# Optimization experiments

Hardware: AMD Instinct MI355X
Metric: run time of the kernel (lower is better)

The kernel has to match this reference:

```python
import jax, jax.numpy as jnp
import numpy as np

BN_EPS = 1e-5

def conv1x1(x, w, b):
    # x: [B,C,H,W], w: [O,C], b: [O] -> [B,O,H,W]
    return jnp.einsum('bchw,oc->bohw', x, w) + b[None, :, None, None]

def maxpool2x2(x):
    B, C, H, W = x.shape
    return x.reshape(B, C, H // 2, 2, W // 2, 2).max(axis=(3, 5))

def setup_inputs() -> dict:
    key = jax.random.key(0)
    ks = jax.random.split(key, 8)
    B, C, Ci, H, W = 16, 256, 128, 64, 64
    s_in = np.sqrt(2.0 / C).astype(np.float32)   # kaiming fan_out-ish scale
    s_out = np.sqrt(2.0 / Ci).astype(np.float32)
    return {
        'inp0': jax.random.normal(ks[0], (1,), jnp.float32),
        'x': jax.random.normal(ks[1], (B, C, H, W), jnp.float32),
        'g_w': jax.random.normal(ks[2], (Ci, C), jnp.float32) * s_in,
        'g_b': jnp.zeros((Ci,), jnp.float32),
        'theta_w': jax.random.normal(ks[3], (Ci, C), jnp.float32) * s_in,
        'theta_b': jnp.zeros((Ci,), jnp.float32),
        'phi_w': jax.random.normal(ks[4], (Ci, C), jnp.float32) * s_in,
        'phi_b': jnp.zeros((Ci,), jnp.float32),
        'W_w': jax.random.normal(ks[5], (C, Ci), jnp.float32) * s_out,
        'W_b': jnp.zeros((C,), jnp.float32),
        'bn_gamma': jnp.ones((C,), jnp.float32),
        'bn_beta': jnp.zeros((C,), jnp.float32),
    }

def reference(inp0, x, g_w, g_b, theta_w, theta_b, phi_w, phi_b, W_w, W_b, bn_gamma, bn_beta):
    B, C, H, W = x.shape
    Ci = g_w.shape[0]
    # g and phi are conv1x1 followed by 2x2 maxpool (sub_sample=True)
    g_x = maxpool2x2(conv1x1(x, g_w, g_b)).reshape(B, Ci, -1)        # [B,Ci,N']
    g_x = g_x.transpose(0, 2, 1)                                      # [B,N',Ci]
    theta_x = conv1x1(x, theta_w, theta_b).reshape(B, Ci, -1)         # [B,Ci,N]
    theta_x = theta_x.transpose(0, 2, 1)                              # [B,N,Ci]
    phi_x = maxpool2x2(conv1x1(x, phi_w, phi_b)).reshape(B, Ci, -1)   # [B,Ci,N']
    f = jnp.einsum('bnc,bcm->bnm', theta_x, phi_x)                    # [B,N,N'] (no scaling)
    f_div_C = jax.nn.softmax(f, axis=-1)
    y = jnp.einsum('bnm,bmc->bnc', f_div_C, g_x)                      # [B,N,Ci]
    y = y.transpose(0, 2, 1).reshape(B, Ci, H, W)
    W_y = conv1x1(y, W_w, W_b)                                        # [B,C,H,W]
    # BatchNorm2d in training mode: batch statistics (biased var), eps=1e-5
    mean = W_y.mean(axis=(0, 2, 3))
    var = W_y.var(axis=(0, 2, 3))
    W_y = (W_y - mean[None, :, None, None]) * jax.lax.rsqrt(var + BN_EPS)[None, :, None, None]
    W_y = W_y * bn_gamma[None, :, None, None] + bn_beta[None, :, None, None]
    z = W_y + x
    # original returns list(inputs[:index]) + [z] + list(inputs[index+1:])
    return (inp0, z)
```

## Files before the change

### kernel.cpp

```cpp
#include <hip/hip_runtime.h>
#include <stdint.h>

typedef __attribute__((ext_vector_type(4))) float f32x4;
typedef __attribute__((ext_vector_type(8))) short s16x8;

__device__ __forceinline__ unsigned short bf16_rne(float f) {
    union { float f; unsigned u; } v; v.f = f;
    return (unsigned short)((v.u + 0x7fffu + ((v.u >> 16) & 1u)) >> 16);
}
__device__ __forceinline__ float bf16_to_f32(unsigned short h) {
    union { unsigned u; float f; } v; v.u = ((unsigned)h) << 16;
    return v.f;
}

__device__ __forceinline__ void async_copy16(unsigned short* lds, const unsigned short* glb) {
    __builtin_amdgcn_global_load_lds(
        (const __attribute__((address_space(1))) unsigned int*)(glb),
        (__attribute__((address_space(3))) unsigned int*)(lds),
        16, 0, 0);
}


template<int MODE>
__global__ __launch_bounds__(256) void conv_kernel(
    const float* __restrict__ x,
    const float* __restrict__ w,
    const float* __restrict__ bias,
    unsigned short* __restrict__ outH,
    unsigned short* __restrict__ outL)
{
    const int b   = blockIdx.y;
    const int n0  = blockIdx.x * 128;
    const int tid = threadIdx.x;
    const int wv  = tid >> 6;
    const int l   = tid & 63;
    const int lg  = l >> 4;
    const int lc  = l & 15;

    __shared__ __align__(16) unsigned short Ah[128][40];
    __shared__ __align__(16) unsigned short Al[128][40];

    f32x4 acc[8][2];
#pragma unroll
    for (int i = 0; i < 8; i++)
#pragma unroll
        for (int j = 0; j < 2; j++) acc[i][j] = (f32x4){0.f, 0.f, 0.f, 0.f};

    for (int kc = 0; kc < 256; kc += 32) {
        __syncthreads();
#pragma unroll
        for (int i = 0; i < 16; i++) {
            int lin = i * 256 + tid;
            int cc  = lin >> 7;
            int nn  = lin & 127;
            float v = x[((size_t)b * 256 + (kc + cc)) * 4096 + n0 + nn];
            unsigned short h = bf16_rne(v);
            Ah[nn][cc] = h;
            if (MODE != 2) Al[nn][cc] = bf16_rne(v - bf16_to_f32(h));
        }
        __syncthreads();

        s16x8 wh[2], wl[2];
#pragma unroll
        for (int ot = 0; ot < 2; ot++) {
            int orow = wv * 32 + ot * 16 + lc;
            const float* wp = w + (size_t)orow * 256 + kc + lg * 8;
#pragma unroll
            for (int j = 0; j < 8; j++) {
                float wvv = wp[j];
                unsigned short h = bf16_rne(wvv);
                wh[ot][j] = (short)h;
                if (MODE != 2) wl[ot][j] = (short)bf16_rne(wvv - bf16_to_f32(h));
            }
        }

#pragma unroll
        for (int mt = 0; mt < 8; mt++) {
            s16x8 ah = *(const s16x8*)&Ah[mt * 16 + lc][lg * 8];
            s16x8 al;
            if (MODE != 2) al = *(const s16x8*)&Al[mt * 16 + lc][lg * 8];
#pragma unroll
            for (int ot = 0; ot < 2; ot++) {
                acc[mt][ot] = __builtin_amdgcn_mfma_f32_16x16x32_bf16(ah, wh[ot], acc[mt][ot], 0, 0, 0);
                if (MODE != 2) {
                    acc[mt][ot] = __builtin_amdgcn_mfma_f32_16x16x32_bf16(ah, wl[ot], acc[mt][ot], 0, 0, 0);
                    acc[mt][ot] = __builtin_amdgcn_mfma_f32_16x16x32_bf16(al, wh[ot], acc[mt][ot], 0, 0, 0);
                }
            }
        }
    }

    if (MODE == 0) {
#pragma unroll
        for (int mt = 0; mt < 8; mt++)
#pragma unroll
            for (int ot = 0; ot < 2; ot++) {
                int o = wv * 32 + ot * 16 + lc;
                float bs = bias[o];
#pragma unroll
                for (int r = 0; r < 4; r++) {
                    int n = n0 + mt * 16 + lg * 4 + r;
                    float v = acc[mt][ot][r] + bs;
                    unsigned short h = bf16_rne(v);
                    size_t idx = ((size_t)b * 4096 + n) * 128 + o;
                    outH[idx] = h;
                    outL[idx] = bf16_rne(v - bf16_to_f32(h));
                }
            }
    } else {
        const int mbase = blockIdx.x * 32;
#pragma unroll
        for (int mt = 0; mt < 4; mt++)
#pragma unroll
            for (int ot = 0; ot < 2; ot++) {
                int o = wv * 32 + ot * 16 + lc;
                float bs = bias[o];
#pragma unroll
                for (int pair = 0; pair < 2; pair++) {
                    float v = fmaxf(fmaxf(acc[mt][ot][2 * pair], acc[mt][ot][2 * pair + 1]),
                                    fmaxf(acc[mt + 4][ot][2 * pair], acc[mt + 4][ot][2 * pair + 1])) + bs;
                    int pw = mt * 8 + lg * 2 + pair;
                    int m  = mbase + pw;
                    if (MODE == 1) {
                        unsigned short h = bf16_rne(v);
                        size_t idx = ((size_t)b * 1024 + m) * 128 + o;
                        outH[idx] = h;
                        outL[idx] = bf16_rne(v - bf16_to_f32(h));
                    } else {
                        outH[((size_t)b * 128 + o) * 1024 + m] = bf16_rne(v);
                    }
                }
            }
    }
}

__global__ __launch_bounds__(256, 4) void attn_kernel(
    const unsigned short* __restrict__ thH,
    const unsigned short* __restrict__ thL,
    const unsigned short* __restrict__ phH,
    const unsigned short* __restrict__ phL,
    const unsigned short* __restrict__ gp,
    unsigned short* __restrict__ y)
{
    const int fid  = blockIdx.x + (blockIdx.y << 6);
    const int xcd  = fid & 7;
    const int slot = fid >> 3;
    const int b    = 2 * xcd + (slot >> 6);
    const int n0   = (slot & 63) * 64;

    const int tid = threadIdx.x;
    const int wv  = tid >> 6;
    const int l   = tid & 63;
    const int lg  = l >> 4;
    const int lc  = l & 15;

    __shared__ __align__(16) unsigned short Kh[2][32 * 128];
    __shared__ __align__(16) unsigned short Kl[2][32 * 128];
    __shared__ __align__(16) unsigned short Pb[4][16 * 40];

    const unsigned short* phHb = phH + (size_t)b * 1024 * 128;
    const unsigned short* phLb = phL + (size_t)b * 1024 * 128;
    const unsigned short* gpb  = gp  + (size_t)b * 128 * 1024;
    unsigned short* Pw = Pb[wv];

    s16x8 qh[4], ql[4];
    {
        const size_t qrow = ((size_t)b * 4096 + n0 + wv * 16 + lc) * 128;
#pragma unroll
        for (int ks = 0; ks < 4; ks++) {
            qh[ks] = *(const s16x8*)(thH + qrow + ks * 32 + lg * 8);
            ql[ks] = *(const s16x8*)(thL + qrow + ks * 32 + lg * 8);
        }
    }

    f32x4 O[8];
#pragma unroll
    for (int t = 0; t < 8; t++) O[t] = (f32x4){0.f, 0.f, 0.f, 0.f};
    float mrun[4] = {-1e30f, -1e30f, -1e30f, -1e30f};
    float lrun[4] = {0.f, 0.f, 0.f, 0.f};

    const int lr  = l >> 4;
    const int sc_ = l & 15;

#define STAGE(buf, kt_)                                                              \
    {                                                                                \
        _Pragma("unroll")                                                            \
        for (int t = 0; t < 2; t++) {                                                \
            int Rt = wv * 8 + t * 4;                                                 \
            int R  = Rt + lr;                                                        \
            int ck = sc_ ^ (R & 15);                                                 \
            size_t src = ((size_t)((kt_) * 32 + R)) * 128 + ck * 8;                  \
            async_copy16(&Kh[buf][Rt * 128], phHb + src);                            \
            async_copy16(&Kl[buf][Rt * 128], phLb + src);                            \
        }                                                                            \
    }

    STAGE(0, 0);

    for (int kt = 0; kt < 32; kt++) {
        const int cur = kt & 1;
        __syncthreads();
        if (kt < 31) STAGE(cur ^ 1, kt + 1);

        const unsigned short* KhT = Kh[cur];
        const unsigned short* KlT = Kl[cur];

        f32x4 s[2];
#pragma unroll
        for (int ct = 0; ct < 2; ct++) s[ct] = (f32x4){0.f, 0.f, 0.f, 0.f};
#pragma unroll
        for (int ct = 0; ct < 2; ct++) {
            const int row = ct * 16 + lc;
#pragma unroll
            for (int ks = 0; ks < 4; ks++) {
                const int slt = (ks * 4 + lg) ^ lc;
                s16x8 kh = *(const s16x8*)(KhT + row * 128 + slt * 8);
                s16x8 kl = *(const s16x8*)(KlT + row * 128 + slt * 8);
                s[ct] = __builtin_amdgcn_mfma_f32_16x16x32_bf16(qh[ks], kh, s[ct], 0, 0, 0);
                s[ct] = __builtin_amdgcn_mfma_f32_16x16x32_bf16(qh[ks], kl, s[ct], 0, 0, 0);
                s[ct] = __builtin_amdgcn_mfma_f32_16x16x32_bf16(ql[ks], kh, s[ct], 0, 0, 0);
            }
        }

        float tm[4];
#pragma unroll
        for (int r = 0; r < 4; r++) tm[r] = fmaxf(s[0][r], s[1][r]);
#pragma unroll
        for (int d = 1; d < 16; d <<= 1)
#pragma unroll
            for (int r = 0; r < 4; r++) tm[r] = fmaxf(tm[r], __shfl_xor(tm[r], d, 64));

        bool grow = (tm[0] > mrun[0]) || (tm[1] > mrun[1]) ||
                    (tm[2] > mrun[2]) || (tm[3] > mrun[3]);
        if (__any(grow)) {
            float scv[4];
#pragma unroll
            for (int r = 0; r < 4; r++) {
                float mn = fmaxf(mrun[r], tm[r]);
                scv[r] = __expf(mrun[r] - mn);
                mrun[r] = mn;
                lrun[r] *= scv[r];
            }
#pragma unroll
            for (int t = 0; t < 8; t++)
#pragma unroll
                for (int r = 0; r < 4; r++) O[t][r] *= scv[r];
        }

        float ts[4] = {0.f, 0.f, 0.f, 0.f};
#pragma unroll
        for (int ct = 0; ct < 2; ct++)
#pragma unroll
            for (int r = 0; r < 4; r++) {
                float e = __expf(s[ct][r] - mrun[r]);
                s[ct][r] = e;
                ts[r] += e;
            }
#pragma unroll
        for (int d = 1; d < 16; d <<= 1)
#pragma unroll
            for (int r = 0; r < 4; r++) ts[r] += __shfl_xor(ts[r], d, 64);
#pragma unroll
        for (int r = 0; r < 4; r++) lrun[r] += ts[r];

#pragma unroll
        for (int ct = 0; ct < 2; ct++)
#pragma unroll
            for (int r = 0; r < 4; r++)
                Pw[(lg * 4 + r) * 40 + ct * 16 + lc] = bf16_rne(s[ct][r]);

        const int mt = kt * 32;
        s16x8 pa = *(const s16x8*)(Pw + lc * 40 + lg * 8);
#pragma unroll
        for (int ci_t = 0; ci_t < 8; ci_t++) {
            s16x8 vb = *(const s16x8*)(gpb + (size_t)(ci_t * 16 + lc) * 1024 + mt + lg * 8);
            O[ci_t] = __builtin_amdgcn_mfma_f32_16x16x32_bf16(pa, vb, O[ci_t], 0, 0, 0);
        }
    }

#pragma unroll
    for (int r = 0; r < 4; r++) {
        float inv = 1.0f / lrun[r];
        int n = n0 + wv * 16 + lg * 4 + r;
        size_t base = ((size_t)b * 4096 + n) * 128;
#pragma unroll
        for (int ci_t = 0; ci_t < 8; ci_t++)
            y[base + ci_t * 16 + lc] = bf16_rne(O[ci_t][r] * inv);
    }
#undef STAGE
}

__global__ __launch_bounds__(256) void wconv_kernel(
    const unsigned short* __restrict__ y,
    const float* __restrict__ Ww,
    const float* __restrict__ Wb,
    unsigned short* __restrict__ wy)
{
    const int b   = blockIdx.z;
    const int o0  = blockIdx.x * 64;
    const int nb  = blockIdx.y * 256;
    const int tid = threadIdx.x;
    const int wv  = tid >> 6;
    const int l   = tid & 63;
    const int lg  = l >> 4;
    const int lc  = l & 15;
    const int n0  = nb + wv * 64;

    f32x4 acc[4][4];
#pragma unroll
    for (int i = 0; i < 4; i++)
#pragma unroll
        for (int j = 0; j < 4; j++) acc[i][j] = (f32x4){0.f, 0.f, 0.f, 0.f};

#pragma unroll
    for (int ks = 0; ks < 4; ks++) {
        s16x8 a[4];
#pragma unroll
        for (int ot = 0; ot < 4; ot++) {
            const float* wp = Ww + (size_t)(o0 + ot * 16 + lc) * 128 + ks * 32 + lg * 8;
#pragma unroll
            for (int j = 0; j < 8; j++) a[ot][j] = (short)bf16_rne(wp[j]);
        }
#pragma unroll
        for (int nt = 0; nt < 4; nt++) {
            s16x8 bf = *(const s16x8*)(y + ((size_t)b * 4096 + n0 + nt * 16 + lc) * 128 + ks * 32 + lg * 8);
#pragma unroll
            for (int ot = 0; ot < 4; ot++)
                acc[ot][nt] = __builtin_amdgcn_mfma_f32_16x16x32_bf16(a[ot], bf, acc[ot][nt], 0, 0, 0);
        }
    }
#pragma unroll
    for (int ot = 0; ot < 4; ot++) {
#pragma unroll
        for (int r = 0; r < 4; r++) {
            int o = o0 + ot * 16 + lg * 4 + r;
            float bsv = Wb[o];
#pragma unroll
            for (int nt = 0; nt < 4; nt++) {
                float v = acc[ot][nt][r] + bsv;
                wy[((size_t)b * 256 + o) * 4096 + n0 + nt * 16 + lc] = bf16_rne(v);
            }
        }
    }
}

__global__ __launch_bounds__(256) void stats_kernel(
    const unsigned short* __restrict__ wy,
    const float* __restrict__ gamma, const float* __restrict__ beta,
    float* __restrict__ scale, float* __restrict__ shift)
{
    const int o = blockIdx.x;
    const int t = threadIdx.x;
    float s1 = 0.f, s2 = 0.f;
    for (int b = 0; b < 16; b++) {
        const unsigned short* p = wy + ((size_t)b * 256 + o) * 4096;
#pragma unroll
        for (int i = 0; i < 4; i++) {
            uint2 u = *(const uint2*)(p + i * 1024 + t * 4);
            float v0 = bf16_to_f32((unsigned short)(u.x & 0xffff));
            float v1 = bf16_to_f32((unsigned short)(u.x >> 16));
            float v2 = bf16_to_f32((unsigned short)(u.y & 0xffff));
            float v3 = bf16_to_f32((unsigned short)(u.y >> 16));
            s1 += v0 + v1 + v2 + v3;
            s2 += v0 * v0 + v1 * v1 + v2 * v2 + v3 * v3;
        }
    }
#pragma unroll
    for (int d = 1; d < 64; d <<= 1) { s1 += __shfl_xor(s1, d, 64); s2 += __shfl_xor(s2, d, 64); }
    __shared__ float rs1[4], rs2[4];
    if ((t & 63) == 0) { rs1[t >> 6] = s1; rs2[t >> 6] = s2; }
    __syncthreads();
    if (t == 0) {
        float S1 = rs1[0] + rs1[1] + rs1[2] + rs1[3];
        float S2 = rs2[0] + rs2[1] + rs2[2] + rs2[3];
        const float cnt = 16.0f * 4096.0f;
        float mean = S1 / cnt;
        float var  = S2 / cnt - mean * mean;
        float sc = gamma[o] * rsqrtf(var + 1e-5f);
        scale[o] = sc;
        shift[o] = beta[o] - mean * sc;
    }
}

__global__ __launch_bounds__(256) void final_kernel(
    const unsigned short* __restrict__ wy,
    const float* __restrict__ x,
    const float* __restrict__ scale, const float* __restrict__ shift,
    const float* __restrict__ inp0,
    float* __restrict__ out)
{
    if (blockIdx.x == 0 && threadIdx.x == 0) out[0] = inp0[0];
    float* z = out + 1;
    const size_t total4 = (size_t)16 * 256 * 4096 / 4;
    for (size_t v = (size_t)blockIdx.x * 256 + threadIdx.x; v < total4; v += (size_t)gridDim.x * 256) {
        size_t e = v * 4;
        int c = (int)((e >> 12) & 255);
        uint2 u = *(const uint2*)(wy + e);
        float4 xv = *(const float4*)(x + e);
        float sc = scale[c], sh = shift[c];
        float z0 = sc * bf16_to_f32((unsigned short)(u.x & 0xffff)) + sh + xv.x;
        float z1 = sc * bf16_to_f32((unsigned short)(u.x >> 16))    + sh + xv.y;
        float z2 = sc * bf16_to_f32((unsigned short)(u.y & 0xffff)) + sh + xv.z;
        float z3 = sc * bf16_to_f32((unsigned short)(u.y >> 16))    + sh + xv.w;
        z[e + 0] = z0; z[e + 1] = z1; z[e + 2] = z2; z[e + 3] = z3;
    }
}

extern "C" void kernel_launch(void* const* d_in, const int* in_sizes, int n_in,
                              void* d_out, int out_size, void* d_ws, size_t ws_size,
                              hipStream_t stream) {
    const float* inp0  = (const float*)d_in[0];
    const float* x     = (const float*)d_in[1];
    const float* g_w   = (const float*)d_in[2];
    const float* g_b   = (const float*)d_in[3];
    const float* th_w  = (const float*)d_in[4];
    const float* th_b  = (const float*)d_in[5];
    const float* ph_w  = (const float*)d_in[6];
    const float* ph_b  = (const float*)d_in[7];
    const float* W_w   = (const float*)d_in[8];
    const float* W_b   = (const float*)d_in[9];
    const float* gamma = (const float*)d_in[10];
    const float* beta  = (const float*)d_in[11];

    char* ws = (char*)d_ws;
    const size_t MB = 1048576;
    unsigned short* thH = (unsigned short*)(ws);
    unsigned short* thL = (unsigned short*)(ws + 16 * MB);
    unsigned short* phH = (unsigned short*)(ws + 32 * MB);
    unsigned short* phL = (unsigned short*)(ws + 36 * MB);
    unsigned short* gpv = (unsigned short*)(ws + 40 * MB);
    unsigned short* yv  = (unsigned short*)(ws + 44 * MB);
    unsigned short* wy  = (unsigned short*)(ws + 60 * MB);
    float* scaleb       = (float*)(ws + 92 * MB);
    float* shiftb       = (float*)(ws + 92 * MB + 1024);

    conv_kernel<0><<<dim3(32, 16), 256, 0, stream>>>(x, th_w, th_b, thH, thL);
    conv_kernel<1><<<dim3(32, 16), 256, 0, stream>>>(x, ph_w, ph_b, phH, phL);
    conv_kernel<2><<<dim3(32, 16), 256, 0, stream>>>(x, g_w, g_b, gpv, gpv);
    attn_kernel<<<dim3(64, 16), 256, 0, stream>>>(thH, thL, phH, phL, gpv, yv);
    wconv_kernel<<<dim3(4, 16, 16), 256, 0, stream>>>(yv, W_w, W_b, wy);
    stats_kernel<<<dim3(256), 256, 0, stream>>>(wy, gamma, beta, scaleb, shiftb);
    final_kernel<<<dim3(2048), 256, 0, stream>>>(wy, x, scaleb, shiftb, inp0, (float*)d_out);
}
```

Measured before the change: 418.8 us.

## Transpose score MFMA operands so softmax row reductions need fewer shuffles

New measurement: 402.0 us. 1.04x faster.

```diff
diff --git a/kernel.cpp b/kernel.cpp
--- a/kernel.cpp
+++ b/kernel.cpp
@@ -49,14 +49,20 @@
     for (int kc = 0; kc < 256; kc += 32) {
         __syncthreads();
 #pragma unroll
-        for (int i = 0; i < 16; i++) {
+        for (int i = 0; i < 8; i++) {
             int lin = i * 256 + tid;
-            int cc  = lin >> 7;
+            int cp  = lin >> 7;
             int nn  = lin & 127;
-            float v = x[((size_t)b * 256 + (kc + cc)) * 4096 + n0 + nn];
-            unsigned short h = bf16_rne(v);
-            Ah[nn][cc] = h;
-            if (MODE != 2) Al[nn][cc] = bf16_rne(v - bf16_to_f32(h));
+            const float* xp = x + ((size_t)b * 256 + (kc + 2 * cp)) * 4096 + n0 + nn;
+            float v0 = xp[0];
+            float v1 = xp[4096];
+            unsigned short h0 = bf16_rne(v0), h1 = bf16_rne(v1);
+            *(unsigned*)&Ah[nn][2 * cp] = (unsigned)h0 | ((unsigned)h1 << 16);
+            if (MODE != 2) {
+                unsigned short l0 = bf16_rne(v0 - bf16_to_f32(h0));
+                unsigned short l1 = bf16_rne(v1 - bf16_to_f32(h1));
+                *(unsigned*)&Al[nn][2 * cp] = (unsigned)l0 | ((unsigned)l1 << 16);
+            }
         }
         __syncthreads();
 
@@ -176,8 +182,8 @@
     f32x4 O[8];
 #pragma unroll
     for (int t = 0; t < 8; t++) O[t] = (f32x4){0.f, 0.f, 0.f, 0.f};
-    float mrun[4] = {-1e30f, -1e30f, -1e30f, -1e30f};
-    float lrun[4] = {0.f, 0.f, 0.f, 0.f};
+    float mrun = -1e30f;
+    float lrun = 0.f;
 
     const int lr  = l >> 4;
     const int sc_ = l & 15;
@@ -216,58 +222,52 @@
                 const int slt = (ks * 4 + lg) ^ lc;
                 s16x8 kh = *(const s16x8*)(KhT + row * 128 + slt * 8);
                 s16x8 kl = *(const s16x8*)(KlT + row * 128 + slt * 8);
-                s[ct] = __builtin_amdgcn_mfma_f32_16x16x32_bf16(qh[ks], kh, s[ct], 0, 0, 0);
-                s[ct] = __builtin_amdgcn_mfma_f32_16x16x32_bf16(qh[ks], kl, s[ct], 0, 0, 0);
-                s[ct] = __builtin_amdgcn_mfma_f32_16x16x32_bf16(ql[ks], kh, s[ct], 0, 0, 0);
-            }
-        }
-
-        float tm[4];
-#pragma unroll
-        for (int r = 0; r < 4; r++) tm[r] = fmaxf(s[0][r], s[1][r]);
-#pragma unroll
-        for (int d = 1; d < 16; d <<= 1)
-#pragma unroll
-            for (int r = 0; r < 4; r++) tm[r] = fmaxf(tm[r], __shfl_xor(tm[r], d, 64));
-
-        bool grow = (tm[0] > mrun[0]) || (tm[1] > mrun[1]) ||
-                    (tm[2] > mrun[2]) || (tm[3] > mrun[3]);
-        if (__any(grow)) {
-            float scv[4];
+                s[ct] = __builtin_amdgcn_mfma_f32_16x16x32_bf16(kh, qh[ks], s[ct], 0, 0, 0);
+                s[ct] = __builtin_amdgcn_mfma_f32_16x16x32_bf16(kl, qh[ks], s[ct], 0, 0, 0);
+                s[ct] = __builtin_amdgcn_mfma_f32_16x16x32_bf16(kh, ql[ks], s[ct], 0, 0, 0);
+            }
+        }
+
+        float tm = fmaxf(fmaxf(fmaxf(s[0][0], s[0][1]), fmaxf(s[0][2], s[0][3])),
+                         fmaxf(fmaxf(s[1][0], s[1][1]), fmaxf(s[1][2], s[1][3])));
+        tm = fmaxf(tm, __shfl_xor(tm, 16, 64));
+        tm = fmaxf(tm, __shfl_xor(tm, 32, 64));
+
+        if (__any(tm > mrun)) {
+            float mn  = fmaxf(mrun, tm);
+            float scr = __expf(mrun - mn);
+            mrun = mn;
+            lrun *= scr;
+            float scO[4];
+#pragma unroll
+            for (int r = 0; r < 4; r++) scO[r] = __shfl(scr, lg * 4 + r, 64);
+#pragma unroll
+            for (int t = 0; t < 8; t++)
+#pragma unroll
+                for (int r = 0; r < 4; r++) O[t][r] *= scO[r];
+        }
+
+        float ts = 0.f;
+        float p[8];
+#pragma unroll
+        for (int ct = 0; ct < 2; ct++)
 #pragma unroll
             for (int r = 0; r < 4; r++) {
-                float mn = fmaxf(mrun[r], tm[r]);
-                scv[r] = __expf(mrun[r] - mn);
-                mrun[r] = mn;
-                lrun[r] *= scv[r];
-            }
-#pragma unroll
-            for (int t = 0; t < 8; t++)
-#pragma unroll
-                for (int r = 0; r < 4; r++) O[t][r] *= scv[r];
-        }
-
-        float ts[4] = {0.f, 0.f, 0.f, 0.f};
-#pragma unroll
-        for (int ct = 0; ct < 2; ct++)
-#pragma unroll
-            for (int r = 0; r < 4; r++) {
-                float e = __expf(s[ct][r] - mrun[r]);
-                s[ct][r] = e;
-                ts[r] += e;
-            }
-#pragma unroll
-        for (int d = 1; d < 16; d <<= 1)
-#pragma unroll
-            for (int r = 0; r < 4; r++) ts[r] += __shfl_xor(ts[r], d, 64);
-#pragma unroll
-        for (int r = 0; r < 4; r++) lrun[r] += ts[r];
-
-#pragma unroll
-        for (int ct = 0; ct < 2; ct++)
-#pragma unroll
-            for (int r = 0; r < 4; r++)
-                Pw[(lg * 4 + r) * 40 + ct * 16 + lc] = bf16_rne(s[ct][r]);
+                float e = __expf(s[ct][r] - mrun);
+                p[ct * 4 + r] = e;
+                ts += e;
+            }
+        ts += __shfl_xor(ts, 16, 64);
+        ts += __shfl_xor(ts, 32, 64);
+        lrun += ts;
+
+#pragma unroll
+        for (int ct = 0; ct < 2; ct++) {
+            unsigned w0 = (unsigned)bf16_rne(p[ct * 4 + 0]) | ((unsigned)bf16_rne(p[ct * 4 + 1]) << 16);
+            unsigned w1 = (unsigned)bf16_rne(p[ct * 4 + 2]) | ((unsigned)bf16_rne(p[ct * 4 + 3]) << 16);
+            uint2 pk; pk.x = w0; pk.y = w1;
+            *(uint2*)&Pw[lc * 40 + ct * 16 + lg * 4] = pk;
+        }
 
         const int mt = kt * 32;
         s16x8 pa = *(const s16x8*)(Pw + lc * 40 + lg * 8);
@@ -278,14 +278,19 @@
         }
     }
 
+    float invO[4];
 #pragma unroll
     for (int r = 0; r < 4; r++) {
-        float inv = 1.0f / lrun[r];
+        float lr_ = __shfl(lrun, lg * 4 + r, 64);
+        invO[r] = 1.0f / lr_;
+    }
+#pragma unroll
+    for (int r = 0; r < 4; r++) {
         int n = n0 + wv * 16 + lg * 4 + r;
         size_t base = ((size_t)b * 4096 + n) * 128;
 #pragma unroll
         for (int ci_t = 0; ci_t < 8; ci_t++)
-            y[base + ci_t * 16 + lc] = bf16_rne(O[ci_t][r] * inv);
+            y[base + ci_t * 16 + lc] = bf16_rne(O[ci_t][r] * invO[r]);
     }
 #undef STAGE
 }
```
